# Kernel tuning notes

Measured on AMD Instinct MI355X. Metric: run time of the kernel, lower is better.

## Reference

```python
import jax, jax.numpy as jnp
import numpy as np

B, LQ, LV = 32, 64, 128
QS, FS, BN = 512, 1024, 512

def setup_inputs() -> dict:
    key = jax.random.key(0)
    k1, k2, k3, k4, k5 = jax.random.split(key, 5)
    s = lambda n: 1.0 / np.sqrt(n)
    return {
        "phr_feats": jax.random.normal(k1, (B, LQ, QS), dtype=jnp.float32),
        "vis_feats": jax.random.normal(k2, (B, LV, FS), dtype=jnp.float32),
        "W": jax.random.uniform(k3, (BN, QS), jnp.float32, -s(QS), s(QS)),
        "U": jax.random.uniform(k4, (BN, FS), jnp.float32, -s(FS), s(FS)),
        "b": jnp.ones((BN,), dtype=jnp.float32),
        "w": jax.random.uniform(k5, (1, BN), jnp.float32, -s(BN), s(BN)),
    }

def reference(phr_feats, vis_feats, W, U, b, w):
    # Wh: [B,Lq,BN], Uv: [B,Lv,BN]
    Wh = jnp.einsum('bqd,nd->bqn', phr_feats, W)
    Uv = jnp.einsum('bvf,nf->bvn', vis_feats, U)
    # broadcast add + tanh: [B,Lq,Lv,BN]
    t = jnp.tanh(Wh[:, :, None, :] + Uv[:, None, :, :] + b)
    energies = jnp.einsum('bqvn,n->bqv', t, w[0])  # squeeze(-1)
    weights = jax.nn.softmax(energies, axis=2)
    aligned = jnp.einsum('bqv,bvf->bqf', weights, vis_feats)
    semantic_group_feats = jnp.concatenate([phr_feats, aligned], axis=2)
    return (semantic_group_feats, weights, energies)
```

## Files before the change

### kernel.cpp

```cpp
#include <hip/hip_runtime.h>

#define NB  32
#define NLQ 64
#define NLV 128
#define NQS 512
#define NFS 1024
#define NBN 512
#define CC  2.8853900817779268f

typedef float  floatx4 __attribute__((ext_vector_type(4)));
typedef __bf16 bf16x8  __attribute__((ext_vector_type(8)));
typedef unsigned short us;

__device__ __forceinline__ us f2bf(float f) {
    unsigned int u = __float_as_uint(f);
    u += 0x7fffu + ((u >> 16) & 1u);
    return (us)(u >> 16);
}
__device__ __forceinline__ unsigned int pktrunc(float lo, float hi) {
    return __builtin_amdgcn_perm(__float_as_uint(hi), __float_as_uint(lo), 0x07060302u);
}
__device__ __forceinline__ float blo(unsigned int u) {
    return __uint_as_float(u << 16);
}
__device__ __forceinline__ float bhi(unsigned int u) {
    return __uint_as_float(u & 0xffff0000u);
}

#define PHR4 262144
#define VIS4 1048576
#define WW4  65536
#define UU4  131072
#define TOT4 (PHR4 + VIS4 + WW4 + UU4)

__global__ __launch_bounds__(256) void convert_bf16(
    const float* __restrict__ phr, const float* __restrict__ vis,
    const float* __restrict__ W,   const float* __restrict__ U,
    us* __restrict__ phr_b, us* __restrict__ vis_b,
    us* __restrict__ W_b,   us* __restrict__ U_b,
    float* __restrict__ out_sgf)
{
    int i = blockIdx.x * 256 + threadIdx.x;
    if (i >= TOT4) return;
    const float* src; us* dst; int o;
    if (i < PHR4)              { src = phr; dst = phr_b; o = i; }
    else if (i < PHR4 + VIS4)  { src = vis; dst = vis_b; o = i - PHR4; }
    else if (i < PHR4 + VIS4 + WW4) { src = W; dst = W_b; o = i - PHR4 - VIS4; }
    else                       { src = U; dst = U_b; o = i - PHR4 - VIS4 - WW4; }
    float4 v = ((const float4*)src)[o];
    uint2 r = { pktrunc(v.x, v.y), pktrunc(v.z, v.w) };
    *(uint2*)(dst + (size_t)o * 4) = r;
    if (i < PHR4) {
        int row = o >> 7, c4 = o & 127;
        ((float4*)out_sgf)[(size_t)row * 384 + c4] = v;
    }
}

__device__ __forceinline__ void gemm64(
    us* As, us* Bs,
    const us* __restrict__ A, const us* __restrict__ Bt,
    const float* __restrict__ bias, us* __restrict__ C,
    int K, int bx, int by, int hasb)
{
    const int tid  = threadIdx.x;
    const int m0   = bx * 64;
    const int n0   = by * 64;
    const int wave = tid >> 6;
    const int lane = tid & 63;
    const int wm   = (wave >> 1) * 32;
    const int wn   = (wave & 1) * 32;
    const int srow = tid >> 2;
    const int sk   = (tid & 3) * 8;
    const int fm   = lane & 15;
    const int fko  = (lane >> 4) * 8;

    floatx4 acc[2][2] = {};
    const us* ag = A  + (size_t)(m0 + srow) * K + sk;
    const us* bg = Bt + (size_t)(n0 + srow) * K + sk;

    uint4 av = *(const uint4*)(ag);
    uint4 bv = *(const uint4*)(bg);

    for (int k0 = 0; k0 < K; k0 += 32) {
        __syncthreads();
        *(uint4*)(As + srow * 40 + sk) = av;
        *(uint4*)(Bs + srow * 40 + sk) = bv;
        const int kn = k0 + 32;
        if (kn < K) {
            av = *(const uint4*)(ag + kn);
            bv = *(const uint4*)(bg + kn);
        }
        __syncthreads();
        bf16x8 am[2], bn[2];
        #pragma unroll
        for (int i = 0; i < 2; ++i)
            am[i] = *(const bf16x8*)(As + (wm + 16 * i + fm) * 40 + fko);
        #pragma unroll
        for (int j = 0; j < 2; ++j)
            bn[j] = *(const bf16x8*)(Bs + (wn + 16 * j + fm) * 40 + fko);
        #pragma unroll
        for (int i = 0; i < 2; ++i)
            #pragma unroll
            for (int j = 0; j < 2; ++j)
                acc[i][j] = __builtin_amdgcn_mfma_f32_16x16x32_bf16(am[i], bn[j], acc[i][j], 0, 0, 0);
    }

    const int cr = (lane >> 4) * 4;
    const int cc = lane & 15;
    #pragma unroll
    for (int i = 0; i < 2; ++i)
        #pragma unroll
        for (int j = 0; j < 2; ++j)
            #pragma unroll
            for (int r = 0; r < 4; ++r) {
                int gm = m0 + wm + 16 * i + cr + r;
                int gn = n0 + wn + 16 * j + cc;
                float v = acc[i][j][r];
                if (hasb) v += bias[gn];
                C[(size_t)gm * NBN + gn] = f2bf(__builtin_amdgcn_exp2f(CC * v));
            }
}

__global__ __launch_bounds__(256) void gemm_both(
    const us* __restrict__ phr_b, const us* __restrict__ W_b,
    const float* __restrict__ bias,
    const us* __restrict__ vis_b, const us* __restrict__ U_b,
    us* __restrict__ whY, us* __restrict__ uvY)
{
    __shared__ __align__(16) us As[64 * 40];
    __shared__ __align__(16) us Bs[64 * 40];
    int blk = blockIdx.x;
    if (blk < 256) {
        gemm64(As, Bs, phr_b, W_b, bias, whY, NQS, blk % 32, blk / 32, 1);
    } else {
        blk -= 256;
        gemm64(As, Bs, vis_b, U_b, bias, uvY, NFS, blk % 64, blk / 64, 0);
    }
}

__global__ __launch_bounds__(256) void energize(
    const us* __restrict__ whY,
    const us* __restrict__ uvY,
    const float* __restrict__ wvec,
    float* __restrict__ p_ws, float* __restrict__ out_w, float* __restrict__ out_e)
{
    const float LOG2E = 1.4426950408889634f;
    const int blk  = blockIdx.x;
    const int q    = blk >> 5;
    const int b    = blk & 31;
    const int row  = b * NLQ + q;
    const int tid  = threadIdx.x;
    const int wave = tid >> 6;
    const int lane = tid & 63;

    __shared__ float e_s[128];

    const int n0 = lane << 3;
    uint4 yq4 = *(const uint4*)(whY + (size_t)row * NBN + n0);
    float Yq[8] = { blo(yq4.x), bhi(yq4.x), blo(yq4.y), bhi(yq4.y),
                    blo(yq4.z), bhi(yq4.z), blo(yq4.w), bhi(yq4.w) };
    float4 w0 = *(const float4*)(wvec + n0);
    float4 w1 = *(const float4*)(wvec + n0 + 4);
    float nw2[8] = { 2.f*w0.x, 2.f*w0.y, 2.f*w0.z, 2.f*w0.w,
                     2.f*w1.x, 2.f*w1.y, 2.f*w1.z, 2.f*w1.w };
    float sumw = w0.x + w0.y + w0.z + w0.w + w1.x + w1.y + w1.z + w1.w;
    #pragma unroll
    for (int off = 32; off; off >>= 1) sumw += __shfl_xor(sumw, off);

    #pragma unroll
    for (int vblk = 0; vblk < 4; ++vblk) {
        const us* base = uvY + ((size_t)b * NLV + wave * 32 + vblk * 8) * NBN + n0;
        float s[8];
        #pragma unroll
        for (int j = 0; j < 8; ++j) {
            uint4 u = *(const uint4*)(base + (size_t)j * NBN);
            float acc = 0.f;
            auto term = [&](unsigned int uu, int k) {
                float d0 = fmaf(blo(uu), Yq[k],     1.f);
                float d1 = fmaf(bhi(uu), Yq[k + 1], 1.f);
                acc = fmaf(nw2[k],     __builtin_amdgcn_rcpf(d0), acc);
                acc = fmaf(nw2[k + 1], __builtin_amdgcn_rcpf(d1), acc);
            };
            term(u.x, 0); term(u.y, 2); term(u.z, 4); term(u.w, 6);
            s[j] = acc;
        }
        #pragma unroll
        for (int m = 8; m <= 32; m <<= 1)
            #pragma unroll
            for (int j = 0; j < 8; ++j) s[j] += __shfl_xor(s[j], m);
        float t[4];
        #pragma unroll
        for (int p = 0; p < 4; ++p) {
            float ae = s[2*p]     + __shfl_xor(s[2*p],     1);
            float bo = s[2*p + 1] + __shfl_xor(s[2*p + 1], 1);
            t[p] = (lane & 1) ? bo : ae;
        }
        float u2[2];
        #pragma unroll
        for (int p = 0; p < 2; ++p) {
            float ae = t[2*p]     + __shfl_xor(t[2*p],     2);
            float bo = t[2*p + 1] + __shfl_xor(t[2*p + 1], 2);
            u2[p] = (lane & 2) ? bo : ae;
        }
        {
            float ae = u2[0] + __shfl_xor(u2[0], 4);
            float bo = u2[1] + __shfl_xor(u2[1], 4);
            float r  = (lane & 4) ? bo : ae;
            if (lane < 8) e_s[wave * 32 + vblk * 8 + lane] = sumw - r;
        }
    }
    __syncthreads();

    if (wave == 0) {
        float e0 = e_s[lane];
        float e1 = e_s[lane + 64];
        float m = fmaxf(e0, e1);
        #pragma unroll
        for (int off = 32; off; off >>= 1) m = fmaxf(m, __shfl_xor(m, off));
        float x0 = __builtin_amdgcn_exp2f((e0 - m) * LOG2E);
        float x1 = __builtin_amdgcn_exp2f((e1 - m) * LOG2E);
        float ss = x0 + x1;
        #pragma unroll
        for (int off = 32; off; off >>= 1) ss += __shfl_xor(ss, off);
        float inv = __builtin_amdgcn_rcpf(ss);
        float p0 = x0 * inv, p1 = x1 * inv;
        size_t o = (size_t)row * NLV;
        p_ws[o + lane]       = p0;
        p_ws[o + lane + 64]  = p1;
        out_w[o + lane]      = p0;
        out_w[o + lane + 64] = p1;
        out_e[o + lane]      = e0;
        out_e[o + lane + 64] = e1;
    }
}

__global__ __launch_bounds__(256) void aligned_k(
    const us* __restrict__ vis_b,
    const float* __restrict__ p_ws,
    float* __restrict__ out_sgf)
{
    const int blk = blockIdx.x;
    const int b   = blk & 31;
    const int qg  = blk >> 5;
    const int tid = threadIdx.x;

    __shared__ float p_s[4][128];
    if (tid < 128) {
        const float* src = p_ws + (size_t)(b * NLQ + qg * 4) * NLV;
        ((float4*)&p_s[0][0])[tid] = ((const float4*)src)[tid];
    }
    __syncthreads();

    const int f0 = tid * 4;
    float4 acc[4] = {};
    const us* vb = vis_b + (size_t)b * NLV * NFS + f0;
    for (int v0 = 0; v0 < NLV; v0 += 4) {
        float4 pv[4];
        #pragma unroll
        for (int qq = 0; qq < 4; ++qq) pv[qq] = *(const float4*)&p_s[qq][v0];
        #pragma unroll
        for (int dv = 0; dv < 4; ++dv) {
            uint2 u = *(const uint2*)(vb + (size_t)(v0 + dv) * NFS);
            float x0 = blo(u.x), x1 = bhi(u.x), x2 = blo(u.y), x3 = bhi(u.y);
            #pragma unroll
            for (int qq = 0; qq < 4; ++qq) {
                float p = (dv == 0) ? pv[qq].x : (dv == 1) ? pv[qq].y
                        : (dv == 2) ? pv[qq].z : pv[qq].w;
                acc[qq].x = fmaf(p, x0, acc[qq].x);
                acc[qq].y = fmaf(p, x1, acc[qq].y);
                acc[qq].z = fmaf(p, x2, acc[qq].z);
                acc[qq].w = fmaf(p, x3, acc[qq].w);
            }
        }
    }
    #pragma unroll
    for (int qq = 0; qq < 4; ++qq) {
        size_t row = (size_t)(b * NLQ + qg * 4 + qq);
        *(float4*)(out_sgf + row * (NQS + NFS) + NQS + f0) = acc[qq];
    }
}

extern "C" void kernel_launch(void* const* d_in, const int* in_sizes, int n_in,
                              void* d_out, int out_size, void* d_ws, size_t ws_size,
                              hipStream_t stream) {
    const float* phr  = (const float*)d_in[0];
    const float* vis  = (const float*)d_in[1];
    const float* W    = (const float*)d_in[2];
    const float* U    = (const float*)d_in[3];
    const float* bias = (const float*)d_in[4];
    const float* wvec = (const float*)d_in[5];

    char* ws = (char*)d_ws;
    us* phr_b = (us*)ws;
    us* vis_b = (us*)(ws + (2u << 20));
    us* W_b   = (us*)(ws + (10u << 20));
    us* U_b   = (us*)(ws + (10u << 20) + (512u << 10));
    us* whY   = (us*)(ws + (12u << 20));
    us* uvY   = (us*)(ws + (14u << 20));
    float* p_ws = (float*)(ws + (18u << 20));

    float* out     = (float*)d_out;
    float* out_sgf = out;
    float* out_w   = out_sgf + (size_t)NB * NLQ * (NQS + NFS);
    float* out_e   = out_w   + (size_t)NB * NLQ * NLV;

    convert_bf16<<<(TOT4 + 255) / 256, 256, 0, stream>>>(
        phr, vis, W, U, phr_b, vis_b, W_b, U_b, out_sgf);
    gemm_both<<<768, 256, 0, stream>>>(phr_b, W_b, bias, vis_b, U_b, whY, uvY);
    energize<<<NB * NLQ, 256, 0, stream>>>(whY, uvY, wvec, p_ws, out_w, out_e);
    aligned_k<<<NB * 16, 256, 0, stream>>>(vis_b, p_ws, out_sgf);
}
```

Measured before the change: 132.9 us.

## Remap energize lanes to 32-wide N chunks with shorter shuffle reductions

The energize kernel now gives each lane a 32-element slice of the bottleneck dimension, with 16 lanes per visual row and 4 rows handled per wave pass. This replaces the long multi-stage cross-lane butterfly reduction over 8 rows with a 4-step shuffle per row, and keeps Yq and w in registers. It also adds a 4-blocks-per-CU launch bound, and drops the duplicate softmax-weight scratch buffer so the next kernel reads out_w directly. The trade-off is more registers per thread (64 floats held), and the new occupancy hint may force register spilling.

```diff
diff --git a/kernel.cpp b/kernel.cpp
--- a/kernel.cpp
+++ b/kernel.cpp
@@ -138,11 +138,11 @@
     }
 }
 
-__global__ __launch_bounds__(256) void energize(
+__global__ __launch_bounds__(256, 4) void energize(
     const us* __restrict__ whY,
     const us* __restrict__ uvY,
     const float* __restrict__ wvec,
-    float* __restrict__ p_ws, float* __restrict__ out_w, float* __restrict__ out_e)
+    float* __restrict__ out_w, float* __restrict__ out_e)
 {
     const float LOG2E = 1.4426950408889634f;
     const int blk  = blockIdx.x;
@@ -152,62 +152,65 @@
     const int tid  = threadIdx.x;
     const int wave = tid >> 6;
     const int lane = tid & 63;
+    const int nl   = lane & 15;
+    const int vl   = lane >> 4;
+    const int n0   = nl << 5;
 
     __shared__ float e_s[128];
 
-    const int n0 = lane << 3;
-    uint4 yq4 = *(const uint4*)(whY + (size_t)row * NBN + n0);
-    float Yq[8] = { blo(yq4.x), bhi(yq4.x), blo(yq4.y), bhi(yq4.y),
-                    blo(yq4.z), bhi(yq4.z), blo(yq4.w), bhi(yq4.w) };
-    float4 w0 = *(const float4*)(wvec + n0);
-    float4 w1 = *(const float4*)(wvec + n0 + 4);
-    float nw2[8] = { 2.f*w0.x, 2.f*w0.y, 2.f*w0.z, 2.f*w0.w,
-                     2.f*w1.x, 2.f*w1.y, 2.f*w1.z, 2.f*w1.w };
-    float sumw = w0.x + w0.y + w0.z + w0.w + w1.x + w1.y + w1.z + w1.w;
+    float Yq[32], w[32];
+    {
+        const us* yqp = whY + (size_t)row * NBN + n0;
+        #pragma unroll
+        for (int i = 0; i < 4; ++i) {
+            uint4 t = *(const uint4*)(yqp + i * 8);
+            Yq[i*8+0]=blo(t.x); Yq[i*8+1]=bhi(t.x);
+            Yq[i*8+2]=blo(t.y); Yq[i*8+3]=bhi(t.y);
+            Yq[i*8+4]=blo(t.z); Yq[i*8+5]=bhi(t.z);
+            Yq[i*8+6]=blo(t.w); Yq[i*8+7]=bhi(t.w);
+        }
+        #pragma unroll
+        for (int i = 0; i < 8; ++i) {
+            float4 t = *(const float4*)(wvec + n0 + i * 4);
+            w[i*4+0]=t.x; w[i*4+1]=t.y; w[i*4+2]=t.z; w[i*4+3]=t.w;
+        }
+    }
+    float sumw = 0.f;
     #pragma unroll
-    for (int off = 32; off; off >>= 1) sumw += __shfl_xor(sumw, off);
-
+    for (int i = 0; i < 32; ++i) sumw += w[i];
     #pragma unroll
-    for (int vblk = 0; vblk < 4; ++vblk) {
-        const us* base = uvY + ((size_t)b * NLV + wave * 32 + vblk * 8) * NBN + n0;
-        float s[8];
-        #pragma unroll
-        for (int j = 0; j < 8; ++j) {
-            uint4 u = *(const uint4*)(base + (size_t)j * NBN);
-            float acc = 0.f;
-            auto term = [&](unsigned int uu, int k) {
-                float d0 = fmaf(blo(uu), Yq[k],     1.f);
-                float d1 = fmaf(bhi(uu), Yq[k + 1], 1.f);
-                acc = fmaf(nw2[k],     __builtin_amdgcn_rcpf(d0), acc);
-                acc = fmaf(nw2[k + 1], __builtin_amdgcn_rcpf(d1), acc);
-            };
-            term(u.x, 0); term(u.y, 2); term(u.z, 4); term(u.w, 6);
-            s[j] = acc;
-        }
-        #pragma unroll
-        for (int m = 8; m <= 32; m <<= 1)
-            #pragma unroll
-            for (int j = 0; j < 8; ++j) s[j] += __shfl_xor(s[j], m);
-        float t[4];
-        #pragma unroll
-        for (int p = 0; p < 4; ++p) {
-            float ae = s[2*p]     + __shfl_xor(s[2*p],     1);
-            float bo = s[2*p + 1] + __shfl_xor(s[2*p + 1], 1);
-            t[p] = (lane & 1) ? bo : ae;
-        }
-        float u2[2];
-        #pragma unroll
-        for (int p = 0; p < 2; ++p) {
-            float ae = t[2*p]     + __shfl_xor(t[2*p],     2);
-            float bo = t[2*p + 1] + __shfl_xor(t[2*p + 1], 2);
-            u2[p] = (lane & 2) ? bo : ae;
-        }
-        {
-            float ae = u2[0] + __shfl_xor(u2[0], 4);
-            float bo = u2[1] + __shfl_xor(u2[1], 4);
-            float r  = (lane & 4) ? bo : ae;
-            if (lane < 8) e_s[wave * 32 + vblk * 8 + lane] = sumw - r;
-        }
+    for (int m = 1; m <= 8; m <<= 1) sumw += __shfl_xor(sumw, m);
+
+    #pragma unroll 2
+    for (int pass = 0; pass < 8; ++pass) {
+        const int v = wave * 32 + pass * 4 + vl;
+        const us* uvp = uvY + ((size_t)b * NLV + v) * NBN + n0;
+        float s0 = 0.f, s1 = 0.f;
+        #pragma unroll
+        for (int i = 0; i < 4; ++i) {
+            uint4 t = *(const uint4*)(uvp + i * 8);
+            const int k = i * 8;
+            float d0 = fmaf(blo(t.x), Yq[k+0], 1.f);
+            float d1 = fmaf(bhi(t.x), Yq[k+1], 1.f);
+            float d2 = fmaf(blo(t.y), Yq[k+2], 1.f);
+            float d3 = fmaf(bhi(t.y), Yq[k+3], 1.f);
+            float d4 = fmaf(blo(t.z), Yq[k+4], 1.f);
+            float d5 = fmaf(bhi(t.z), Yq[k+5], 1.f);
+            float d6 = fmaf(blo(t.w), Yq[k+6], 1.f);
+            float d7 = fmaf(bhi(t.w), Yq[k+7], 1.f);
+            s0 = fmaf(w[k+0], __builtin_amdgcn_rcpf(d0), s0);
+            s1 = fmaf(w[k+1], __builtin_amdgcn_rcpf(d1), s1);
+            s0 = fmaf(w[k+2], __builtin_amdgcn_rcpf(d2), s0);
+            s1 = fmaf(w[k+3], __builtin_amdgcn_rcpf(d3), s1);
+            s0 = fmaf(w[k+4], __builtin_amdgcn_rcpf(d4), s0);
+            s1 = fmaf(w[k+5], __builtin_amdgcn_rcpf(d5), s1);
+            s0 = fmaf(w[k+6], __builtin_amdgcn_rcpf(d6), s0);
+            s1 = fmaf(w[k+7], __builtin_amdgcn_rcpf(d7), s1);
+        }
+        float s = s0 + s1;
+        #pragma unroll
+        for (int m = 1; m <= 8; m <<= 1) s += __shfl_xor(s, m);
+        if (nl == 0) e_s[v] = fmaf(-2.f, s, sumw);
     }
     __syncthreads();
 
@@ -225,8 +228,6 @@
         float inv = __builtin_amdgcn_rcpf(ss);
         float p0 = x0 * inv, p1 = x1 * inv;
         size_t o = (size_t)row * NLV;
-        p_ws[o + lane]       = p0;
-        p_ws[o + lane + 64]  = p1;
         out_w[o + lane]      = p0;
         out_w[o + lane + 64] = p1;
         out_e[o + lane]      = e0;
@@ -236,7 +237,7 @@
 
 __global__ __launch_bounds__(256) void aligned_k(
     const us* __restrict__ vis_b,
-    const float* __restrict__ p_ws,
+    const float* __restrict__ p_w,
     float* __restrict__ out_sgf)
 {
     const int blk = blockIdx.x;
@@ -246,7 +247,7 @@
 
     __shared__ float p_s[4][128];
     if (tid < 128) {
-        const float* src = p_ws + (size_t)(b * NLQ + qg * 4) * NLV;
+        const float* src = p_w + (size_t)(b * NLQ + qg * 4) * NLV;
         ((float4*)&p_s[0][0])[tid] = ((const float4*)src)[tid];
     }
     __syncthreads();
@@ -297,7 +298,6 @@
     us* U_b   = (us*)(ws + (10u << 20) + (512u << 10));
     us* whY   = (us*)(ws + (12u << 20));
     us* uvY   = (us*)(ws + (14u << 20));
-    float* p_ws = (float*)(ws + (18u << 20));
 
     float* out     = (float*)d_out;
     float* out_sgf = out;
@@ -307,6 +307,6 @@
     convert_bf16<<<(TOT4 + 255) / 256, 256, 0, stream>>>(
         phr, vis, W, U, phr_b, vis_b, W_b, U_b, out_sgf);
     gemm_both<<<768, 256, 0, stream>>>(phr_b, W_b, bias, vis_b, U_b, whY, uvY);
-    energize<<<NB * NLQ, 256, 0, stream>>>(whY, uvY, wvec, p_ws, out_w, out_e);
-    aligned_k<<<NB * 16, 256, 0, stream>>>(vis_b, p_ws, out_sgf);
-}
+    energize<<<NB * NLQ, 256, 0, stream>>>(whY, uvY, wvec, out_w, out_e);
+    aligned_k<<<NB * 16, 256, 0, stream>>>(vis_b, out_w, out_sgf);
+}
```

Result: slower. 138.9 us (+4.5%).
